# Kernel tuning notes

Measured on AMD Instinct MI355X. Metric: run time of the kernel, lower is better.

The kernel has to match this reference:

```python
import jax, jax.numpy as jnp
import numpy as np


def setup_inputs() -> dict:
    key = jax.random.key(0)
    k1, k2, k3, k4 = jax.random.split(key, 4)
    B = 1048576        # batch of annotator ids
    A = 65536          # num_annotators
    D = 8              # latent_dims
    annotator = jax.random.randint(k1, (B,), 0, A, dtype=jnp.int64)
    posterior_mu = jax.random.normal(k2, (A, D), dtype=jnp.float32)
    posterior_covtril = jax.random.normal(k3, (A, D, D), dtype=jnp.float32)
    eps = jax.random.normal(k4, (B, D), dtype=jnp.float32)
    return {
        "annotator": annotator,
        "posterior_mu": posterior_mu,
        "posterior_covtril": posterior_covtril,
        "eps": eps,
    }


def reference(annotator, posterior_mu, posterior_covtril, eps):
    # Batched equivalent of the per-annotator MVN rsample loop:
    #   z_i = mu[a_i] + tril(covtril[a_i]) @ eps_i
    mu = posterior_mu[annotator]                 # [B, D]   gather
    L = jnp.tril(posterior_covtril[annotator])   # [B, D, D] gather + tril mask
    z = mu + jnp.einsum("bij,bj->bi", L, eps)    # reparameterized sample
    return z
```

## Files before the change

### kernel.cpp

```cpp
#include <hip/hip_runtime.h>
#include <hip/hip_bf16.h>
#include <hip/hip_fp16.h>


typedef float    f32x4 __attribute__((ext_vector_type(4)));
typedef _Float16 f16x8 __attribute__((ext_vector_type(8)));

__device__ __constant__ const int SL_SRC[28] = {
    8, 16,17, 24,25,26, 32,33,34,35, 40,41,42,43,44,
    48,49,50,51,52,53, 56,57,58,59,60,61,62
};
__device__ __constant__ const int DIAG_SRC[8] = {0,9,18,27,36,45,54,63};

__global__ __launch_bounds__(256) void pack_kernel(
    const float* __restrict__ mu,
    const float* __restrict__ L,
    _Float16* __restrict__ rec,
    int A)
{
    int a = blockIdx.x * blockDim.x + threadIdx.x;
    if (a >= A) return;

    const f32x4* muv = reinterpret_cast<const f32x4*>(mu + (size_t)a * 8);
    const f32x4* Lv  = reinterpret_cast<const f32x4*>(L + (size_t)a * 64);
    f32x4 m0 = __builtin_nontemporal_load(muv);
    f32x4 m1 = __builtin_nontemporal_load(muv + 1);
    f32x4 r[16];
    #pragma unroll
    for (int k = 0; k < 16; ++k) r[k] = __builtin_nontemporal_load(Lv + k);

    f16x8 ch[6];
    #pragma unroll
    for (int k = 0; k < 28; ++k) {
        const int f = SL_SRC[k];
        ch[k >> 3][k & 7] = (_Float16)r[f >> 2][f & 3];
    }
    #pragma unroll
    for (int i = 0; i < 8; ++i) {
        const int k = 28 + i;
        const float v = (i < 4) ? m0[i] : m1[i - 4];
        ch[k >> 3][k & 7] = (_Float16)v;
    }
    #pragma unroll
    for (int i = 0; i < 8; ++i) {
        const int k = 36 + i;
        const int f = DIAG_SRC[i];
        ch[k >> 3][k & 7] = (_Float16)r[f >> 2][f & 3];
    }
    #pragma unroll
    for (int k = 44; k < 48; ++k) ch[k >> 3][k & 7] = (_Float16)0.f;

    f16x8* o = reinterpret_cast<f16x8*>(rec + (size_t)a * 48);
    #pragma unroll
    for (int c = 0; c < 6; ++c) __builtin_nontemporal_store(ch[c], o + c);
}

#define ROWS 4

__global__ __launch_bounds__(256) void lv_main(
    const int* __restrict__ ann,
    const _Float16* __restrict__ rec,
    const float* __restrict__ eps,
    float* __restrict__ out,
    int B)
{
    const int tid = threadIdx.x;
    const long base = (long)blockIdx.x * (256 * ROWS);

    long row[ROWS];
    int a[ROWS];
    #pragma unroll
    for (int k = 0; k < ROWS; ++k) {
        row[k] = base + k * 256 + tid;
        a[k] = (row[k] < (long)B) ? __builtin_nontemporal_load(ann + row[k]) : 0;
    }

    f16x8 ch[ROWS][6];
    #pragma unroll
    for (int k = 0; k < ROWS; ++k) {
        const f16x8* rp = reinterpret_cast<const f16x8*>(rec + (size_t)a[k] * 48);
        #pragma unroll
        for (int c = 0; c < 6; ++c) ch[k][c] = rp[c];
    }

    f32x4 ev0[ROWS], ev1[ROWS];
    #pragma unroll
    for (int k = 0; k < ROWS; ++k) {
        const long rc = (row[k] < (long)B) ? row[k] : 0;
        const f32x4* ep = reinterpret_cast<const f32x4*>(eps + (size_t)rc * 8);
        ev0[k] = __builtin_nontemporal_load(ep);
        ev1[k] = __builtin_nontemporal_load(ep + 1);
    }

    #pragma unroll
    for (int k = 0; k < ROWS; ++k) {
        if (row[k] >= (long)B) continue;
        const float e[8] = {ev0[k][0], ev0[k][1], ev0[k][2], ev0[k][3],
                            ev1[k][0], ev1[k][1], ev1[k][2], ev1[k][3]};
        float z[8];
        #pragma unroll
        for (int i = 0; i < 8; ++i) {
            const int km = 28 + i, kd = 36 + i;
            z[i] = (float)ch[k][km >> 3][km & 7]
                 + (float)ch[k][kd >> 3][kd & 7] * e[i];
        }
        #pragma unroll
        for (int i = 1; i < 8; ++i) {
            const int sb = i * (i - 1) / 2;
            #pragma unroll
            for (int j = 0; j < i; ++j) {
                const int s = sb + j;
                z[i] += (float)ch[k][s >> 3][s & 7] * e[j];
            }
        }
        f32x4* outv = reinterpret_cast<f32x4*>(out + (size_t)row[k] * 8);
        f32x4 o0 = {z[0], z[1], z[2], z[3]};
        f32x4 o1 = {z[4], z[5], z[6], z[7]};
        __builtin_nontemporal_store(o0, outv);
        __builtin_nontemporal_store(o1, outv + 1);
    }
}

__global__ __launch_bounds__(256) void lv_kernel_f32(
    const int* __restrict__ ann,
    const float* __restrict__ mu,
    const float* __restrict__ L,
    const float* __restrict__ eps,
    float* __restrict__ out,
    int B)
{
    int b = blockIdx.x * blockDim.x + threadIdx.x;
    if (b >= B) return;
    const int a = ann[b];
    const f32x4* epsv = reinterpret_cast<const f32x4*>(eps + (size_t)b * 8);
    const f32x4 e0 = epsv[0];
    const f32x4 e1 = epsv[1];
    const float e[8] = {e0[0], e0[1], e0[2], e0[3], e1[0], e1[1], e1[2], e1[3]};
    const f32x4* muv = reinterpret_cast<const f32x4*>(mu + (size_t)a * 8);
    const f32x4 m0 = muv[0];
    const f32x4 m1 = muv[1];
    float z[8] = {m0[0], m0[1], m0[2], m0[3], m1[0], m1[1], m1[2], m1[3]};
    const f32x4* Lv = reinterpret_cast<const f32x4*>(L + (size_t)a * 64);
    #pragma unroll
    for (int i = 0; i < 4; ++i) {
        const f32x4 r0 = Lv[i * 2];
        #pragma unroll
        for (int j = 0; j <= i; ++j) z[i] += r0[j] * e[j];
    }
    #pragma unroll
    for (int i = 4; i < 8; ++i) {
        const f32x4 r0 = Lv[i * 2];
        const f32x4 r1 = Lv[i * 2 + 1];
        const float rr[8] = {r0[0], r0[1], r0[2], r0[3], r1[0], r1[1], r1[2], r1[3]};
        #pragma unroll
        for (int j = 0; j <= i; ++j) z[i] += rr[j] * e[j];
    }
    f32x4* outv = reinterpret_cast<f32x4*>(out + (size_t)b * 8);
    f32x4 o0 = {z[0], z[1], z[2], z[3]};
    f32x4 o1 = {z[4], z[5], z[6], z[7]};
    outv[0] = o0;
    outv[1] = o1;
}

extern "C" void kernel_launch(void* const* d_in, const int* in_sizes, int n_in,
                              void* d_out, int out_size, void* d_ws, size_t ws_size,
                              hipStream_t stream) {
    const int*   ann = (const int*)d_in[0];
    const float* mu  = (const float*)d_in[1];
    const float* L   = (const float*)d_in[2];
    const float* eps = (const float*)d_in[3];
    float* out = (float*)d_out;

    const int B = in_sizes[0];
    const int A = in_sizes[1] / 8;

    const size_t rec_bytes = (size_t)A * 48 * sizeof(_Float16);
    if (ws_size >= rec_bytes) {
        _Float16* rec = (_Float16*)d_ws;
        pack_kernel<<<(A + 255) / 256, 256, 0, stream>>>(mu, L, rec, A);
        const int rows_per_block = 256 * ROWS;
        const int blocks = (B + rows_per_block - 1) / rows_per_block;
        lv_main<<<blocks, 256, 0, stream>>>(ann, rec, eps, out, B);
    } else {
        lv_kernel_f32<<<(B + 255) / 256, 256, 0, stream>>>(ann, mu, L, eps, out, B);
    }
}
```

Before: 50.01 us.

## Fuse pack and gather into one cooperative kernel with grid sync

Merges the pack pass and the gather-compute pass into one cooperative persistent kernel that runs grid-stride loops separated by a grid-wide barrier, so the second launch and its gap disappear. Packed records are padded to 64 halves (128 B) for alignment, rows per thread drop from four to two, and the fallback launches now process 512 rows per block. The host now queries the device, its attributes and occupancy on every call, which adds overhead. The f32 fallback is removed, so the function silently returns without computing when the workspace is too small.

```diff
diff --git a/kernel.cpp b/kernel.cpp
--- a/kernel.cpp
+++ b/kernel.cpp
@@ -1,6 +1,9 @@
 #include <hip/hip_runtime.h>
 #include <hip/hip_bf16.h>
 #include <hip/hip_fp16.h>
+#include <hip/hip_cooperative_groups.h>
+
+namespace cg = cooperative_groups;
 
 
 typedef float    f32x4 __attribute__((ext_vector_type(4)));
@@ -12,15 +15,10 @@
 };
 __device__ __constant__ const int DIAG_SRC[8] = {0,9,18,27,36,45,54,63};
 
-__global__ __launch_bounds__(256) void pack_kernel(
-    const float* __restrict__ mu,
-    const float* __restrict__ L,
-    _Float16* __restrict__ rec,
-    int A)
+__device__ __forceinline__ void pack_one(
+    const float* __restrict__ mu, const float* __restrict__ L,
+    _Float16* __restrict__ rec, int a)
 {
-    int a = blockIdx.x * blockDim.x + threadIdx.x;
-    if (a >= A) return;
-
     const f32x4* muv = reinterpret_cast<const f32x4*>(mu + (size_t)a * 8);
     const f32x4* Lv  = reinterpret_cast<const f32x4*>(L + (size_t)a * 64);
     f32x4 m0 = __builtin_nontemporal_load(muv);
@@ -47,45 +45,33 @@
         const int f = DIAG_SRC[i];
         ch[k >> 3][k & 7] = (_Float16)r[f >> 2][f & 3];
     }
+    f16x8* o = reinterpret_cast<f16x8*>(rec + (size_t)a * 64);
     #pragma unroll
-    for (int k = 44; k < 48; ++k) ch[k >> 3][k & 7] = (_Float16)0.f;
-
-    f16x8* o = reinterpret_cast<f16x8*>(rec + (size_t)a * 48);
-    #pragma unroll
-    for (int c = 0; c < 6; ++c) __builtin_nontemporal_store(ch[c], o + c);
+    for (int c = 0; c < 6; ++c) o[c] = ch[c];
 }
 
-#define ROWS 4
+__device__ __forceinline__ void main_chunk2(
+    const int* __restrict__ ann, const _Float16* __restrict__ rec,
+    const float* __restrict__ eps, float* __restrict__ out,
+    long r0, long r1, int B)
+{
+    long row[2] = {r0, r1};
+    int a[2];
+    #pragma unroll
+    for (int k = 0; k < 2; ++k)
+        a[k] = (row[k] < (long)B) ? __builtin_nontemporal_load(ann + row[k]) : 0;
 
-__global__ __launch_bounds__(256) void lv_main(
-    const int* __restrict__ ann,
-    const _Float16* __restrict__ rec,
-    const float* __restrict__ eps,
-    float* __restrict__ out,
-    int B)
-{
-    const int tid = threadIdx.x;
-    const long base = (long)blockIdx.x * (256 * ROWS);
-
-    long row[ROWS];
-    int a[ROWS];
+    f16x8 ch[2][6];
     #pragma unroll
-    for (int k = 0; k < ROWS; ++k) {
-        row[k] = base + k * 256 + tid;
-        a[k] = (row[k] < (long)B) ? __builtin_nontemporal_load(ann + row[k]) : 0;
-    }
-
-    f16x8 ch[ROWS][6];
-    #pragma unroll
-    for (int k = 0; k < ROWS; ++k) {
-        const f16x8* rp = reinterpret_cast<const f16x8*>(rec + (size_t)a[k] * 48);
+    for (int k = 0; k < 2; ++k) {
+        const f16x8* rp = reinterpret_cast<const f16x8*>(rec + (size_t)a[k] * 64);
         #pragma unroll
         for (int c = 0; c < 6; ++c) ch[k][c] = rp[c];
     }
 
-    f32x4 ev0[ROWS], ev1[ROWS];
+    f32x4 ev0[2], ev1[2];
     #pragma unroll
-    for (int k = 0; k < ROWS; ++k) {
+    for (int k = 0; k < 2; ++k) {
         const long rc = (row[k] < (long)B) ? row[k] : 0;
         const f32x4* ep = reinterpret_cast<const f32x4*>(eps + (size_t)rc * 8);
         ev0[k] = __builtin_nontemporal_load(ep);
@@ -93,7 +79,7 @@
     }
 
     #pragma unroll
-    for (int k = 0; k < ROWS; ++k) {
+    for (int k = 0; k < 2; ++k) {
         if (row[k] >= (long)B) continue;
         const float e[8] = {ev0[k][0], ev0[k][1], ev0[k][2], ev0[k][3],
                             ev1[k][0], ev1[k][1], ev1[k][2], ev1[k][3]};
@@ -121,67 +107,77 @@
     }
 }
 
-__global__ __launch_bounds__(256) void lv_kernel_f32(
-    const int* __restrict__ ann,
-    const float* __restrict__ mu,
-    const float* __restrict__ L,
-    const float* __restrict__ eps,
-    float* __restrict__ out,
-    int B)
+__global__ __launch_bounds__(256, 4) void lv_fused(
+    const int* __restrict__ ann, const float* __restrict__ mu,
+    const float* __restrict__ L, const float* __restrict__ eps,
+    float* __restrict__ out, _Float16* __restrict__ rec, int B, int A)
 {
-    int b = blockIdx.x * blockDim.x + threadIdx.x;
-    if (b >= B) return;
-    const int a = ann[b];
-    const f32x4* epsv = reinterpret_cast<const f32x4*>(eps + (size_t)b * 8);
-    const f32x4 e0 = epsv[0];
-    const f32x4 e1 = epsv[1];
-    const float e[8] = {e0[0], e0[1], e0[2], e0[3], e1[0], e1[1], e1[2], e1[3]};
-    const f32x4* muv = reinterpret_cast<const f32x4*>(mu + (size_t)a * 8);
-    const f32x4 m0 = muv[0];
-    const f32x4 m1 = muv[1];
-    float z[8] = {m0[0], m0[1], m0[2], m0[3], m1[0], m1[1], m1[2], m1[3]};
-    const f32x4* Lv = reinterpret_cast<const f32x4*>(L + (size_t)a * 64);
-    #pragma unroll
-    for (int i = 0; i < 4; ++i) {
-        const f32x4 r0 = Lv[i * 2];
-        #pragma unroll
-        for (int j = 0; j <= i; ++j) z[i] += r0[j] * e[j];
-    }
-    #pragma unroll
-    for (int i = 4; i < 8; ++i) {
-        const f32x4 r0 = Lv[i * 2];
-        const f32x4 r1 = Lv[i * 2 + 1];
-        const float rr[8] = {r0[0], r0[1], r0[2], r0[3], r1[0], r1[1], r1[2], r1[3]};
-        #pragma unroll
-        for (int j = 0; j <= i; ++j) z[i] += rr[j] * e[j];
-    }
-    f32x4* outv = reinterpret_cast<f32x4*>(out + (size_t)b * 8);
-    f32x4 o0 = {z[0], z[1], z[2], z[3]};
-    f32x4 o1 = {z[4], z[5], z[6], z[7]};
-    outv[0] = o0;
-    outv[1] = o1;
+    const int nth = gridDim.x * blockDim.x;
+    const int tid = blockIdx.x * blockDim.x + threadIdx.x;
+
+    for (int a = tid; a < A; a += nth) pack_one(mu, L, rec, a);
+
+    cg::this_grid().sync();
+
+    for (long s0 = 0; s0 < (long)B; s0 += 2L * nth)
+        main_chunk2(ann, rec, eps, out, s0 + tid, s0 + nth + tid, B);
+}
+
+__global__ __launch_bounds__(256) void pack_kernel(
+    const float* __restrict__ mu, const float* __restrict__ L,
+    _Float16* __restrict__ rec, int A)
+{
+    int a = blockIdx.x * blockDim.x + threadIdx.x;
+    if (a < A) pack_one(mu, L, rec, a);
+}
+
+__global__ __launch_bounds__(256) void lv_main(
+    const int* __restrict__ ann, const _Float16* __restrict__ rec,
+    const float* __restrict__ eps, float* __restrict__ out, int B)
+{
+    const int tid = threadIdx.x;
+    const long base = (long)blockIdx.x * 512;
+    main_chunk2(ann, rec, eps, out, base + tid, base + 256 + tid, B);
 }
 
 extern "C" void kernel_launch(void* const* d_in, const int* in_sizes, int n_in,
                               void* d_out, int out_size, void* d_ws, size_t ws_size,
                               hipStream_t stream) {
-    const int*   ann = (const int*)d_in[0];
+    const int* ann   = (const int*)d_in[0];
     const float* mu  = (const float*)d_in[1];
     const float* L   = (const float*)d_in[2];
     const float* eps = (const float*)d_in[3];
     float* out = (float*)d_out;
 
-    const int B = in_sizes[0];
-    const int A = in_sizes[1] / 8;
+    int B = in_sizes[0];
+    int A = in_sizes[1] / 8;
 
-    const size_t rec_bytes = (size_t)A * 48 * sizeof(_Float16);
-    if (ws_size >= rec_bytes) {
-        _Float16* rec = (_Float16*)d_ws;
-        pack_kernel<<<(A + 255) / 256, 256, 0, stream>>>(mu, L, rec, A);
-        const int rows_per_block = 256 * ROWS;
-        const int blocks = (B + rows_per_block - 1) / rows_per_block;
-        lv_main<<<blocks, 256, 0, stream>>>(ann, rec, eps, out, B);
-    } else {
-        lv_kernel_f32<<<(B + 255) / 256, 256, 0, stream>>>(ann, mu, L, eps, out, B);
+    const size_t rec_bytes = (size_t)A * 64 * sizeof(_Float16);
+    if (ws_size < rec_bytes) {
+        return;
     }
+    _Float16* rec = (_Float16*)d_ws;
+
+    int dev = 0;
+    hipGetDevice(&dev);
+    int coop = 0;
+    hipDeviceGetAttribute(&coop, hipDeviceAttributeCooperativeLaunch, dev);
+    int ncu = 0;
+    hipDeviceGetAttribute(&ncu, hipDeviceAttributeMultiprocessorCount, dev);
+    int blocksPerCU = 0;
+    hipOccupancyMaxActiveBlocksPerMultiprocessor(&blocksPerCU, lv_fused, 256, 0);
+
+    long maxBlocks = (long)blocksPerCU * (long)ncu;
+    long grid = maxBlocks < 1024 ? maxBlocks : 1024;
+
+    if (coop && grid >= 64) {
+        void* args[] = {(void*)&ann, (void*)&mu, (void*)&L, (void*)&eps,
+                        (void*)&out, (void*)&rec, (void*)&B, (void*)&A};
+        hipError_t st = hipLaunchCooperativeKernel(
+            (const void*)lv_fused, dim3((unsigned)grid), dim3(256), args, 0, stream);
+        if (st == hipSuccess) return;
+    }
+
+    pack_kernel<<<(A + 255) / 256, 256, 0, stream>>>(mu, L, rec, A);
+    lv_main<<<(B + 511) / 512, 256, 0, stream>>>(ann, rec, eps, out, B);
 }
```

Result: slower. 142.0 us (+183.9%).
